# Kernel optimization log

Hardware: AMD Instinct MI355X
Metric: run time of the kernel (lower is better)

Reference implementation:

```python
import jax, jax.numpy as jnp
import numpy as np

NT, NF, CIN, COUT = 1_500_000, 500_000, 32, 32
BN_EPS = 1e-5


def setup_inputs() -> dict:
    key = jax.random.key(0)
    k1, k2, k3 = jax.random.split(key, 3)
    input_texture = jax.random.normal(k1, (NT, CIN), dtype=jnp.float32)
    # barycentric coefficients: nonnegative, rows sum to 1
    b = jax.random.uniform(k2, (NT, 3), dtype=jnp.float32) + 1e-3
    bary_coeff = b / b.sum(axis=1, keepdims=True)
    # 3 texture samples per facet (sum == NT)
    num_texture = jnp.full((NF,), 3, dtype=jnp.int32)
    # xavier-normal init for [Cout, Cin, 3] kernel
    fan = CIN * 3 + COUT * 3
    std = float(np.sqrt(2.0 / fan))
    weights = jax.random.normal(k3, (COUT, CIN, 3), dtype=jnp.float32) * std
    bias = jnp.zeros((1, COUT), dtype=jnp.float32)
    gamma = jnp.ones((COUT,), dtype=jnp.float32)
    beta = jnp.zeros((COUT,), dtype=jnp.float32)
    return {"input_texture": input_texture, "bary_coeff": bary_coeff,
            "num_texture": num_texture, "weights": weights, "bias": bias,
            "gamma": gamma, "beta": beta}


def reference(input_texture, bary_coeff, num_texture, weights, bias, gamma, beta):
    nf = num_texture.shape[0]
    nt = input_texture.shape[0]
    # segment id for each ragged texture sample (original op uses cumsum offsets)
    seg = jnp.repeat(jnp.arange(nf), num_texture, total_repeat_length=nt)
    # per-sample contribution: y[t,o] = sum_{c,k} x[t,c] * b[t,k] * W[o,c,k]
    y = jnp.einsum('tc,tk,ock->to', input_texture, bary_coeff, weights)
    # facet2facet averages over the samples of each facet
    s = jax.ops.segment_sum(y, seg, num_segments=nf)  # [Nf, Cout]
    cnt = jnp.maximum(num_texture.astype(y.dtype), 1)[:, None]
    out = s / cnt
    out = out + bias          # bias add
    out = jax.nn.relu(out)    # activation
    # BatchNorm1d in training mode: batch statistics over the facet dim
    mean = out.mean(axis=0)
    var = out.var(axis=0)
    out = (out - mean) * jax.lax.rsqrt(var + BN_EPS) * gamma + beta
    return out
```

## Files before the change

### kernel.cpp

```cpp
#include <hip/hip_runtime.h>
#include <hip/hip_bf16.h>
#include <stdint.h>

typedef __attribute__((ext_vector_type(4))) float fv4;
typedef __attribute__((ext_vector_type(4))) short sv4;
typedef __attribute__((ext_vector_type(8))) short sv8;

#define SCHUNK 2048
#define FPB 64
#define PZB 108

static __device__ __forceinline__ short f2bf(float f) {
  __hip_bfloat16 h = __float2bfloat16(f);
  union { __hip_bfloat16 h; short s; } u; u.h = h;
  return u.s;
}

__global__ __launch_bounds__(256) void scan1(const int* __restrict__ num, int nf,
                                             int* __restrict__ bsum) {
  __shared__ int sd[256];
  int b = blockIdx.x, tid = threadIdx.x;
  int base = b * SCHUNK + tid * 8;
  int s = 0;
#pragma unroll
  for (int j = 0; j < 8; ++j) { int i = base + j; if (i < nf) s += num[i]; }
  sd[tid] = s; __syncthreads();
  for (int st = 128; st > 0; st >>= 1) {
    if (tid < st) sd[tid] += sd[tid + st];
    __syncthreads();
  }
  if (tid == 0) bsum[b] = sd[0];
}

__global__ __launch_bounds__(256) void scan2(int* __restrict__ bsum, int nb) {
  __shared__ int sd[256];
  int tid = threadIdx.x;
  int v = (tid < nb) ? bsum[tid] : 0;
  sd[tid] = v; __syncthreads();
  for (int off = 1; off < 256; off <<= 1) {
    int t = (tid >= off) ? sd[tid - off] : 0;
    __syncthreads();
    sd[tid] += t;
    __syncthreads();
  }
  if (tid < nb) bsum[tid] = sd[tid] - v;
}

__global__ __launch_bounds__(256) void scan3(const int* __restrict__ num, int nf,
                                             const int* __restrict__ bsum,
                                             int* __restrict__ offsets) {
  __shared__ int sc_[256];
  int b = blockIdx.x, tid = threadIdx.x;
  int base = b * SCHUNK + tid * 8;
  int loc[8]; int s = 0;
#pragma unroll
  for (int j = 0; j < 8; ++j) {
    loc[j] = (base + j < nf) ? num[base + j] : 0;
    s += loc[j];
  }
  sc_[tid] = s; __syncthreads();
  for (int off = 1; off < 256; off <<= 1) {
    int t = (tid >= off) ? sc_[tid - off] : 0;
    __syncthreads();
    sc_[tid] += t;
    __syncthreads();
  }
  int run = bsum[b] + sc_[tid] - s;
#pragma unroll
  for (int j = 0; j < 8; ++j) {
    if (base + j < nf) offsets[base + j] = run;
    run += loc[j];
  }
  if (b == gridDim.x - 1 && tid == 255) offsets[nf] = run;
}

__global__ __launch_bounds__(256) void k_main(
    const float* __restrict__ x, const float* __restrict__ bary,
    const float* __restrict__ W, const float* __restrict__ bias,
    const int* __restrict__ offsets, float* __restrict__ out,
    float* __restrict__ partials, int nf, int nblk)
{
  __shared__ short Z[FPB * PZB];
  __shared__ short W2[32 * PZB];
  __shared__ int off_s[FPB + 1];

  const int tid = threadIdx.x;
  const int f0 = blockIdx.x * FPB;

  for (int idx = tid; idx < 3072; idx += 256) {
    int o = idx / 96;
    int ck = idx - o * 96;
    int k = ck >> 5, c = ck & 31;
    W2[o * PZB + ck] = f2bf(W[o * 96 + c * 3 + k]);
  }
  if (tid < FPB + 1) {
    int f = f0 + tid; if (f > nf) f = nf;
    off_s[tid] = offsets[f];
  }
  __syncthreads();

  {
    const int fl = tid >> 2;
    const int cb = (tid & 3) * 8;
    const int st = off_s[fl], en = off_s[fl + 1];

    float z0[8], z1[8], z2[8];
#pragma unroll
    for (int j = 0; j < 8; ++j) { z0[j] = 0.f; z1[j] = 0.f; z2[j] = 0.f; }

    if (en - st == 3) {
      fv4 xs[3][2];
      float bb[3][3];
#pragma unroll
      for (int s = 0; s < 3; ++s) {
        const float* xp = x + (size_t)(st + s) * 32 + cb;
        xs[s][0] = *(const fv4*)(xp);
        xs[s][1] = *(const fv4*)(xp + 4);
      }
#pragma unroll
      for (int s = 0; s < 3; ++s) {
        const float* bp = bary + (size_t)(st + s) * 3;
        bb[s][0] = bp[0]; bb[s][1] = bp[1]; bb[s][2] = bp[2];
      }
#pragma unroll
      for (int s = 0; s < 3; ++s)
#pragma unroll
        for (int q = 0; q < 2; ++q)
#pragma unroll
          for (int j = 0; j < 4; ++j) {
            float xv = xs[s][q][j];
            z0[q * 4 + j] += xv * bb[s][0];
            z1[q * 4 + j] += xv * bb[s][1];
            z2[q * 4 + j] += xv * bb[s][2];
          }
    } else {
      for (int t = st; t < en; ++t) {
        const float* xp = x + (size_t)t * 32 + cb;
        fv4 xa = *(const fv4*)(xp);
        fv4 xb = *(const fv4*)(xp + 4);
        const float* bp = bary + (size_t)t * 3;
        float b0 = bp[0], b1 = bp[1], b2 = bp[2];
#pragma unroll
        for (int j = 0; j < 4; ++j) {
          z0[j]     += xa[j] * b0; z1[j]     += xa[j] * b1; z2[j]     += xa[j] * b2;
          z0[4 + j] += xb[j] * b0; z1[4 + j] += xb[j] * b1; z2[4 + j] += xb[j] * b2;
        }
      }
    }

    short* zr = &Z[fl * PZB + cb];
#pragma unroll
    for (int g = 0; g < 2; ++g) {
      sv4 p0, p1, p2;
#pragma unroll
      for (int j = 0; j < 4; ++j) {
        p0[j] = f2bf(z0[g * 4 + j]);
        p1[j] = f2bf(z1[g * 4 + j]);
        p2[j] = f2bf(z2[g * 4 + j]);
      }
      *(sv4*)(zr + g * 4)      = p0;
      *(sv4*)(zr + 32 + g * 4) = p1;
      *(sv4*)(zr + 64 + g * 4) = p2;
    }
  }
  __syncthreads();

  const int lane = tid & 63;
  const int wv = tid >> 6;
  const int rowl = lane & 15;
  const int grp = lane >> 4;

  fv4 acc[2];
  acc[0] = (fv4){0.f, 0.f, 0.f, 0.f};
  acc[1] = (fv4){0.f, 0.f, 0.f, 0.f};

#pragma unroll
  for (int kb = 0; kb < 3; ++kb) {
    const int cko = kb * 32 + grp * 4;
    sv8 bfr[2];
#pragma unroll
    for (int n = 0; n < 2; ++n) {
      const short* wr = &W2[(n * 16 + rowl) * PZB + cko];
      sv4 lo = *(const sv4*)(wr);
      sv4 hi = *(const sv4*)(wr + 16);
#pragma unroll
      for (int j = 0; j < 4; ++j) { bfr[n][j] = lo[j]; bfr[n][4 + j] = hi[j]; }
    }
    const short* zr = &Z[(wv * 16 + rowl) * PZB + cko];
    sv4 lo = *(const sv4*)(zr);
    sv4 hi = *(const sv4*)(zr + 16);
    sv8 afr;
#pragma unroll
    for (int j = 0; j < 4; ++j) { afr[j] = lo[j]; afr[4 + j] = hi[j]; }
    acc[0] = __builtin_amdgcn_mfma_f32_16x16x32_bf16(afr, bfr[0], acc[0], 0, 0, 0);
    acc[1] = __builtin_amdgcn_mfma_f32_16x16x32_bf16(afr, bfr[1], acc[1], 0, 0, 0);
  }
  __syncthreads();

  float* yt = (float*)Z;
#pragma unroll
  for (int n = 0; n < 2; ++n)
#pragma unroll
    for (int r = 0; r < 4; ++r)
      yt[(wv * 16 + grp * 4 + r) * 33 + n * 16 + rowl] = acc[n][r];
  __syncthreads();

  const int o_ep = tid & 31;
  const int g_ep = tid >> 5;
  float bo = bias[o_ep];
  float s1 = 0.f, s2 = 0.f;
#pragma unroll
  for (int i = 0; i < 8; ++i) {
    int fl = i * 8 + g_ep;
    int f = f0 + fl;
    if (f < nf) {
      int nm = off_s[fl + 1] - off_s[fl];
      float v = yt[fl * 33 + o_ep] / (float)(nm > 1 ? nm : 1) + bo;
      v = fmaxf(v, 0.f);
      out[f * 32 + o_ep] = v;
      s1 += v; s2 += v * v;
    }
  }
  __syncthreads();
  float* red = (float*)W2;
  red[tid] = s1;
  red[256 + tid] = s2;
  __syncthreads();
  if (tid < 32) {
    float a1 = 0.f, a2 = 0.f;
#pragma unroll
    for (int g = 0; g < 8; ++g) { a1 += red[g * 32 + tid]; a2 += red[256 + g * 32 + tid]; }
    partials[(long)tid * nblk + blockIdx.x]        = a1;
    partials[(long)(32 + tid) * nblk + blockIdx.x] = a2;
  }
}

__global__ __launch_bounds__(256) void k_reduce(const float* __restrict__ partials,
                                                int nblk, float* __restrict__ stats) {
  __shared__ float sd[256];
  int c = blockIdx.x;
  const float* p = partials + (long)c * nblk;
  float s = 0.f;
  for (int i = threadIdx.x; i < nblk; i += 256) s += p[i];
  sd[threadIdx.x] = s; __syncthreads();
  for (int st = 128; st > 0; st >>= 1) {
    if (threadIdx.x < st) sd[threadIdx.x] += sd[threadIdx.x + st];
    __syncthreads();
  }
  if (threadIdx.x == 0) stats[c] = sd[0];
}

__global__ __launch_bounds__(256) void k_bn(float* __restrict__ out,
                                            const float* __restrict__ stats,
                                            const float* __restrict__ gamma,
                                            const float* __restrict__ beta, int nf) {
  __shared__ float sc[32], sh[32];
  if (threadIdx.x < 32) {
    int o = threadIdx.x;
    float inv_n = 1.0f / (float)nf;
    float mean = stats[o] * inv_n;
    float var = stats[32 + o] * inv_n - mean * mean;
    float rstd = rsqrtf(var + 1e-5f);
    float g = gamma[o] * rstd;
    sc[o] = g;
    sh[o] = beta[o] - mean * g;
  }
  __syncthreads();
  long total4 = (long)nf * 8;
  long idx0 = (long)blockIdx.x * 256 + threadIdx.x;
  int ob = ((int)idx0 & 7) * 4;
  fv4 scv = *(const fv4*)&sc[ob];
  fv4 shv = *(const fv4*)&sh[ob];
  for (long idx = idx0; idx < total4; idx += (long)gridDim.x * 256) {
    fv4 v = *((const fv4*)out + idx);
    v = v * scv + shv;
    *((fv4*)out + idx) = v;
  }
}

extern "C" void kernel_launch(void* const* d_in, const int* in_sizes, int n_in,
                              void* d_out, int out_size, void* d_ws, size_t ws_size,
                              hipStream_t stream) {
  const float* x     = (const float*)d_in[0];
  const float* bary  = (const float*)d_in[1];
  const int*   numt  = (const int*)d_in[2];
  const float* W     = (const float*)d_in[3];
  const float* bias  = (const float*)d_in[4];
  const float* gamma = (const float*)d_in[5];
  const float* beta  = (const float*)d_in[6];
  float* out = (float*)d_out;

  const int nf   = in_sizes[2];
  const int nblk = (nf + FPB - 1) / FPB;
  const int nbS  = (nf + SCHUNK - 1) / SCHUNK;

  char* w = (char*)d_ws;
  int* offsets = (int*)w;
  size_t off1 = (4UL * (size_t)(nf + 1) + 255) & ~255UL;
  int* bsum = (int*)(w + off1);
  size_t off2 = (off1 + 4UL * (size_t)nbS + 255) & ~255UL;
  float* partials = (float*)(w + off2);
  size_t off3 = (off2 + 4UL * 64UL * (size_t)nblk + 255) & ~255UL;
  float* stats = (float*)(w + off3);

  scan1<<<nbS, 256, 0, stream>>>(numt, nf, bsum);
  scan2<<<1, 256, 0, stream>>>(bsum, nbS);
  scan3<<<nbS, 256, 0, stream>>>(numt, nf, bsum, offsets);
  k_main<<<nblk, 256, 0, stream>>>(x, bary, W, bias, offsets, out, partials, nf, nblk);
  k_reduce<<<64, 256, 0, stream>>>(partials, nblk, stats);
  k_bn<<<2048, 256, 0, stream>>>(out, stats, gamma, beta, nf);
}
```

Baseline: 109.8 us.

## Make k_main wave-local: precompute bf16 weights, drop block barriers and LDS epilogue

Moves the per-block fp32-to-bf16 weight transposition into a one-off prep kernel and has the MFMA B-fragments read straight from global memory. Each wave now handles its own 16 facets, so the block-wide __syncthreads become a wave barrier and each wave loads its own offsets. The epilogue works directly from MFMA accumulator registers with shuffles, using shuffled sample counts and shuffle-xor reductions, and writes per-wave partials. This removes block barriers, LDS traffic and the redundant per-block weight conversion. In exchange it adds a kernel launch, four times as many partials for k_reduce, and less coalesced output stores.

```diff
diff --git a/kernel.cpp b/kernel.cpp
--- a/kernel.cpp
+++ b/kernel.cpp
@@ -74,41 +74,45 @@
   if (b == gridDim.x - 1 && tid == 255) offsets[nf] = run;
 }
 
+__global__ __launch_bounds__(256) void k_prep(const float* __restrict__ W,
+                                              short* __restrict__ w2g) {
+  for (int i = threadIdx.x; i < 3072; i += 256) {
+    int o = i / 96;
+    int ck = i - o * 96;
+    int k = ck >> 5, c = ck & 31;
+    w2g[o * 96 + ck] = f2bf(W[o * 96 + c * 3 + k]);
+  }
+}
+
 __global__ __launch_bounds__(256) void k_main(
     const float* __restrict__ x, const float* __restrict__ bary,
-    const float* __restrict__ W, const float* __restrict__ bias,
+    const short* __restrict__ w2g, const float* __restrict__ bias,
     const int* __restrict__ offsets, float* __restrict__ out,
-    float* __restrict__ partials, int nf, int nblk)
+    float* __restrict__ partials, int nf, int nw)
 {
-  __shared__ short Z[FPB * PZB];
-  __shared__ short W2[32 * PZB];
-  __shared__ int off_s[FPB + 1];
+  __shared__ short Z[4 * 16 * PZB];
 
   const int tid = threadIdx.x;
-  const int f0 = blockIdx.x * FPB;
-
-  for (int idx = tid; idx < 3072; idx += 256) {
-    int o = idx / 96;
-    int ck = idx - o * 96;
-    int k = ck >> 5, c = ck & 31;
-    W2[o * PZB + ck] = f2bf(W[o * 96 + c * 3 + k]);
-  }
-  if (tid < FPB + 1) {
-    int f = f0 + tid; if (f > nf) f = nf;
-    off_s[tid] = offsets[f];
-  }
-  __syncthreads();
+  const int lane = tid & 63;
+  const int wv = tid >> 6;
+  const int f0 = blockIdx.x * FPB + wv * 16;
+  short* Zw = &Z[wv * 16 * PZB];
+
+  const int fl = lane >> 2;
+  const int cb = (lane & 3) * 8;
+  const int f = f0 + fl;
+  const int fa = f < nf ? f : nf;
+  const int fb = (f + 1) < nf ? (f + 1) : nf;
+  const int st = offsets[fa];
+  const int en = offsets[fb];
+  const int nm_my = en - st;
 
   {
-    const int fl = tid >> 2;
-    const int cb = (tid & 3) * 8;
-    const int st = off_s[fl], en = off_s[fl + 1];
-
     float z0[8], z1[8], z2[8];
 #pragma unroll
     for (int j = 0; j < 8; ++j) { z0[j] = 0.f; z1[j] = 0.f; z2[j] = 0.f; }
 
-    if (en - st == 3) {
+    if (nm_my == 3) {
       fv4 xs[3][2];
       float bb[3][3];
 #pragma unroll
@@ -148,7 +152,7 @@
       }
     }
 
-    short* zr = &Z[fl * PZB + cb];
+    short* zr = &Zw[fl * PZB + cb];
 #pragma unroll
     for (int g = 0; g < 2; ++g) {
       sv4 p0, p1, p2;
@@ -163,10 +167,9 @@
       *(sv4*)(zr + 64 + g * 4) = p2;
     }
   }
-  __syncthreads();
-
-  const int lane = tid & 63;
-  const int wv = tid >> 6;
+
+  __builtin_amdgcn_wave_barrier();
+
   const int rowl = lane & 15;
   const int grp = lane >> 4;
 
@@ -180,13 +183,13 @@
     sv8 bfr[2];
 #pragma unroll
     for (int n = 0; n < 2; ++n) {
-      const short* wr = &W2[(n * 16 + rowl) * PZB + cko];
+      const short* wr = w2g + (n * 16 + rowl) * 96 + cko;
       sv4 lo = *(const sv4*)(wr);
       sv4 hi = *(const sv4*)(wr + 16);
 #pragma unroll
       for (int j = 0; j < 4; ++j) { bfr[n][j] = lo[j]; bfr[n][4 + j] = hi[j]; }
     }
-    const short* zr = &Z[(wv * 16 + rowl) * PZB + cko];
+    const short* zr = &Zw[rowl * PZB + cko];
     sv4 lo = *(const sv4*)(zr);
     sv4 hi = *(const sv4*)(zr + 16);
     sv8 afr;
@@ -195,53 +198,46 @@
     acc[0] = __builtin_amdgcn_mfma_f32_16x16x32_bf16(afr, bfr[0], acc[0], 0, 0, 0);
     acc[1] = __builtin_amdgcn_mfma_f32_16x16x32_bf16(afr, bfr[1], acc[1], 0, 0, 0);
   }
-  __syncthreads();
-
-  float* yt = (float*)Z;
-#pragma unroll
-  for (int n = 0; n < 2; ++n)
-#pragma unroll
-    for (int r = 0; r < 4; ++r)
-      yt[(wv * 16 + grp * 4 + r) * 33 + n * 16 + rowl] = acc[n][r];
-  __syncthreads();
-
-  const int o_ep = tid & 31;
-  const int g_ep = tid >> 5;
-  float bo = bias[o_ep];
-  float s1 = 0.f, s2 = 0.f;
-#pragma unroll
-  for (int i = 0; i < 8; ++i) {
-    int fl = i * 8 + g_ep;
-    int f = f0 + fl;
-    if (f < nf) {
-      int nm = off_s[fl + 1] - off_s[fl];
-      float v = yt[fl * 33 + o_ep] / (float)(nm > 1 ? nm : 1) + bo;
-      v = fmaxf(v, 0.f);
-      out[f * 32 + o_ep] = v;
-      s1 += v; s2 += v * v;
+
+  float bo0 = bias[rowl];
+  float bo1 = bias[16 + rowl];
+  float s1l = 0.f, s1h = 0.f, s2l = 0.f, s2h = 0.f;
+#pragma unroll
+  for (int r = 0; r < 4; ++r) {
+    int row = grp * 4 + r;
+    int fr = f0 + row;
+    int nm = __shfl(nm_my, row * 4, 64);
+    float den = (float)(nm > 1 ? nm : 1);
+    float inv = 1.0f / den;
+    if (fr < nf) {
+      float v0 = fmaxf(acc[0][r] * inv + bo0, 0.f);
+      float v1 = fmaxf(acc[1][r] * inv + bo1, 0.f);
+      out[fr * 32 + rowl]      = v0;
+      out[fr * 32 + 16 + rowl] = v1;
+      s1l += v0; s2l += v0 * v0;
+      s1h += v1; s2h += v1 * v1;
     }
   }
-  __syncthreads();
-  float* red = (float*)W2;
-  red[tid] = s1;
-  red[256 + tid] = s2;
-  __syncthreads();
-  if (tid < 32) {
-    float a1 = 0.f, a2 = 0.f;
-#pragma unroll
-    for (int g = 0; g < 8; ++g) { a1 += red[g * 32 + tid]; a2 += red[256 + g * 32 + tid]; }
-    partials[(long)tid * nblk + blockIdx.x]        = a1;
-    partials[(long)(32 + tid) * nblk + blockIdx.x] = a2;
+  s1l += __shfl_xor(s1l, 16, 64); s1l += __shfl_xor(s1l, 32, 64);
+  s1h += __shfl_xor(s1h, 16, 64); s1h += __shfl_xor(s1h, 32, 64);
+  s2l += __shfl_xor(s2l, 16, 64); s2l += __shfl_xor(s2l, 32, 64);
+  s2h += __shfl_xor(s2h, 16, 64); s2h += __shfl_xor(s2h, 32, 64);
+  if (grp == 0) {
+    int w = blockIdx.x * 4 + wv;
+    partials[(long)(rowl)      * nw + w] = s1l;
+    partials[(long)(16 + rowl) * nw + w] = s1h;
+    partials[(long)(32 + rowl) * nw + w] = s2l;
+    partials[(long)(48 + rowl) * nw + w] = s2h;
   }
 }
 
 __global__ __launch_bounds__(256) void k_reduce(const float* __restrict__ partials,
-                                                int nblk, float* __restrict__ stats) {
+                                                int nw, float* __restrict__ stats) {
   __shared__ float sd[256];
   int c = blockIdx.x;
-  const float* p = partials + (long)c * nblk;
+  const float* p = partials + (long)c * nw;
   float s = 0.f;
-  for (int i = threadIdx.x; i < nblk; i += 256) s += p[i];
+  for (int i = threadIdx.x; i < nw; i += 256) s += p[i];
   sd[threadIdx.x] = s; __syncthreads();
   for (int st = 128; st > 0; st >>= 1) {
     if (threadIdx.x < st) sd[threadIdx.x] += sd[threadIdx.x + st];
@@ -292,6 +288,7 @@
 
   const int nf   = in_sizes[2];
   const int nblk = (nf + FPB - 1) / FPB;
+  const int nw   = nblk * 4;
   const int nbS  = (nf + SCHUNK - 1) / SCHUNK;
 
   char* w = (char*)d_ws;
@@ -299,14 +296,17 @@
   size_t off1 = (4UL * (size_t)(nf + 1) + 255) & ~255UL;
   int* bsum = (int*)(w + off1);
   size_t off2 = (off1 + 4UL * (size_t)nbS + 255) & ~255UL;
-  float* partials = (float*)(w + off2);
-  size_t off3 = (off2 + 4UL * 64UL * (size_t)nblk + 255) & ~255UL;
-  float* stats = (float*)(w + off3);
+  short* w2g = (short*)(w + off2);
+  size_t off3 = (off2 + 2UL * 3072UL + 255) & ~255UL;
+  float* partials = (float*)(w + off3);
+  size_t off4 = (off3 + 4UL * 64UL * (size_t)nw + 255) & ~255UL;
+  float* stats = (float*)(w + off4);
 
   scan1<<<nbS, 256, 0, stream>>>(numt, nf, bsum);
   scan2<<<1, 256, 0, stream>>>(bsum, nbS);
   scan3<<<nbS, 256, 0, stream>>>(numt, nf, bsum, offsets);
-  k_main<<<nblk, 256, 0, stream>>>(x, bary, W, bias, offsets, out, partials, nf, nblk);
-  k_reduce<<<64, 256, 0, stream>>>(partials, nblk, stats);
+  k_prep<<<1, 256, 0, stream>>>(W, w2g);
+  k_main<<<nblk, 256, 0, stream>>>(x, bary, w2g, bias, offsets, out, partials, nf, nw);
+  k_reduce<<<64, 256, 0, stream>>>(partials, nw, stats);
   k_bn<<<2048, 256, 0, stream>>>(out, stats, gamma, beta, nf);
 }
```

After: 143.5 us. 1.31x slower.
